# Performance work log

Measured on AMD Instinct MI355X. Metric: run time of the kernel, lower is better.

## Reference

```python
import jax, jax.numpy as jnp
import numpy as np

NUM_K_HEADS = 16
NUM_V_HEADS = 32
DK = 128
DV = 128
KCONV = 4
EPS = 1e-6
KEY_DIM = NUM_K_HEADS * DK      # 2048
VALUE_DIM = NUM_V_HEADS * DV    # 4096
HIDDEN = 2048
T_TOKENS = 4096


def setup_inputs() -> dict:
    key = jax.random.key(0)
    ks = jax.random.split(key, 10)
    s = 0.02
    return {
        "hidden_states": jax.random.normal(ks[0], (T_TOKENS, HIDDEN), jnp.float32),
        "W_qkv": jax.random.normal(ks[1], (2 * KEY_DIM + VALUE_DIM, HIDDEN), jnp.float32) * s,
        "W_z": jax.random.normal(ks[2], (VALUE_DIM, HIDDEN), jnp.float32) * s,
        "W_b": jax.random.normal(ks[3], (NUM_V_HEADS, HIDDEN), jnp.float32) * s,
        "W_a": jax.random.normal(ks[4], (NUM_V_HEADS, HIDDEN), jnp.float32) * s,
        "conv_weight": jax.random.normal(ks[5], (2 * KEY_DIM + VALUE_DIM, KCONV), jnp.float32) * 0.2,
        "dt_bias": jnp.ones((NUM_V_HEADS,), jnp.float32),
        "A_log": jax.random.normal(ks[6], (NUM_V_HEADS,), jnp.float32) * 0.5,
        "norm_weight": jnp.ones((DV,), jnp.float32),
        "W_out": jax.random.normal(ks[7], (HIDDEN, VALUE_DIM), jnp.float32) * s,
    }


def _l2norm(x):
    return x * jax.lax.rsqrt(jnp.sum(x * x, axis=-1, keepdims=True) + 1e-6)


def _gdn_forward(hidden_states, W_qkv, W_z, W_b, W_a, conv_weight,
                 dt_bias, A_log, norm_weight, W_out):
    T = hidden_states.shape[0]
    # input projections
    mixed_qkv = hidden_states @ W_qkv.T                         # [T, 2K+V]
    z = (hidden_states @ W_z.T).reshape(T, NUM_V_HEADS, DV)     # gate
    b = hidden_states @ W_b.T                                   # [T, Hv]
    a = hidden_states @ W_a.T                                   # [T, Hv]

    # depthwise causal conv1d (kernel 4) + silu, no bias
    xp = jnp.pad(mixed_qkv, ((KCONV - 1, 0), (0, 0)))
    conv = sum(xp[i:i + T] * conv_weight[:, i] for i in range(KCONV))
    x = jax.nn.silu(conv)

    q = x[:, :KEY_DIM].reshape(T, NUM_K_HEADS, DK)
    k = x[:, KEY_DIM:2 * KEY_DIM].reshape(T, NUM_K_HEADS, DK)
    v = x[:, 2 * KEY_DIM:].reshape(T, NUM_V_HEADS, DV)

    rep = NUM_V_HEADS // NUM_K_HEADS  # grouped value attention: repeat q/k heads
    q = jnp.repeat(_l2norm(q), rep, axis=1)  # [T, Hv, DK]
    k = jnp.repeat(_l2norm(k), rep, axis=1)

    beta = jax.nn.sigmoid(b)                                   # [T, Hv]
    g = -jnp.exp(A_log) * jax.nn.softplus(a + dt_bias)         # [T, Hv] log-decay
    scale = DK ** -0.5

    def step(S, inp):
        qt, kt, vt, bt, gt = inp
        S = S * jnp.exp(gt)[:, None, None]                     # gated decay
        kv = jnp.einsum('hk,hkv->hv', kt, S)                   # memory readout
        delta = (vt - kv) * bt[:, None]                        # delta rule update
        S = S + jnp.einsum('hk,hv->hkv', kt, delta)
        ot = jnp.einsum('hk,hkv->hv', qt, S) * scale
        return S, ot

    S0 = jnp.zeros((NUM_V_HEADS, DK, DV), mixed_qkv.dtype)
    _, o = jax.lax.scan(step, S0, (q, k, v, beta, g))          # o: [T, Hv, DV]

    # gated RMSNorm (norm before gate)
    var = jnp.mean(o * o, axis=-1, keepdims=True)
    on = o * jax.lax.rsqrt(var + EPS) * norm_weight
    y = on * jax.nn.silu(z)

    return y.reshape(T, VALUE_DIM) @ W_out.T                   # [T, HIDDEN]


def reference(hidden_states, W_qkv, W_z, W_b, W_a, conv_weight,
              dt_bias, A_log, norm_weight, W_out):
    return _gdn_forward(hidden_states, W_qkv, W_z, W_b, W_a, conv_weight,
                        dt_bias, A_log, norm_weight, W_out)
```

## Files before the change

### kernel.cpp

```cpp
#include <hip/hip_runtime.h>
#include <cstdint>
#include <cstddef>

typedef __bf16 bf16_t;
typedef __bf16 bf16x8 __attribute__((ext_vector_type(8)));
typedef __bf16 bf16x4 __attribute__((ext_vector_type(4)));
typedef float floatx4 __attribute__((ext_vector_type(4)));

__device__ __forceinline__ void async16(const bf16_t* g, bf16_t* l) {
  __builtin_amdgcn_global_load_lds(
      (const __attribute__((address_space(1))) unsigned int*)g,
      (__attribute__((address_space(3))) unsigned int*)l, 16, 0, 0);
}

__device__ __forceinline__ void barrier_lds() {
  asm volatile("s_waitcnt lgkmcnt(0)\n\ts_barrier" ::: "memory");
}

__device__ __forceinline__ float siluf(float x) { return x / (1.f + __expf(-x)); }

#define MFMA16(a, b, c) __builtin_amdgcn_mfma_f32_16x16x32_bf16(a, b, c, 0, 0, 0)

__global__ __launch_bounds__(256) void k_cvt(const float* __restrict__ in,
                                             bf16_t* __restrict__ out, int n4) {
  int i = blockIdx.x * 256 + threadIdx.x;
  if (i >= n4) return;
  const float4 f = ((const float4*)in)[i];
  bf16x4 r;
  r[0] = (bf16_t)f.x; r[1] = (bf16_t)f.y; r[2] = (bf16_t)f.z; r[3] = (bf16_t)f.w;
  ((bf16x4*)out)[i] = r;
}

__global__ __launch_bounds__(256) void k_build_wba(const float* __restrict__ wb,
                                                   const float* __restrict__ wa,
                                                   bf16_t* __restrict__ out) {
  int i = blockIdx.x * 256 + threadIdx.x;
  int e = i * 4;
  int row = e >> 11;
  int col = e & 2047;
  float4 f = make_float4(0.f, 0.f, 0.f, 0.f);
  if (row < 32)      f = *(const float4*)&wb[row * 2048 + col];
  else if (row < 64) f = *(const float4*)&wa[(row - 32) * 2048 + col];
  bf16x4 r;
  r[0] = (bf16_t)f.x; r[1] = (bf16_t)f.y; r[2] = (bf16_t)f.z; r[3] = (bf16_t)f.w;
  *(bf16x4*)&out[e] = r;
}

template<bool OUT_BF16>
__global__ __launch_bounds__(256) void gemm_bt(const bf16_t* __restrict__ A,
                                               const bf16_t* __restrict__ B,
                                               void* __restrict__ Cout,
                                               int M, int N, int K) {
  __shared__ __align__(16) bf16_t As[4096];
  __shared__ __align__(16) bf16_t Bs[4096];
  const int tid  = threadIdx.x;
  const int lane = tid & 63;
  const int wave = tid >> 6;
  const int quad = lane >> 4;
  const int l16  = lane & 15;
  const int wr   = (wave >> 1) * 64;
  const int wc   = (wave & 1) * 64;
  const int m0   = blockIdx.y * 128;
  const int n0   = blockIdx.x * 128;
  const int ra   = tid >> 2;
  const int ca   = (tid & 3) * 8;

  const bf16_t* gA = A + (size_t)(m0 + ra) * K + ca;
  const bf16_t* gB = B + (size_t)(n0 + ra) * K + ca;
  bf16_t* lA = &As[tid * 8];
  bf16_t* lB = &Bs[tid * 8];

  floatx4 acc[4][4] = {};

  for (int k0 = 0; k0 < K; k0 += 32) {
    __syncthreads();
    async16(gA + k0, lA);
    async16(gA + k0 + (size_t)64 * K, lA + 2048);
    async16(gB + k0, lB);
    async16(gB + k0 + (size_t)64 * K, lB + 2048);
    __syncthreads();
    bf16x8 af[4], bfr[4];
#pragma unroll
    for (int i = 0; i < 4; ++i) {
      af[i]  = *(const bf16x8*)&As[(wr + i * 16 + l16) * 32 + quad * 8];
      bfr[i] = *(const bf16x8*)&Bs[(wc + i * 16 + l16) * 32 + quad * 8];
    }
#pragma unroll
    for (int mi = 0; mi < 4; ++mi)
#pragma unroll
      for (int ni = 0; ni < 4; ++ni)
        acc[mi][ni] = MFMA16(af[mi], bfr[ni], acc[mi][ni]);
  }

#pragma unroll
  for (int mi = 0; mi < 4; ++mi) {
#pragma unroll
    for (int ni = 0; ni < 4; ++ni) {
      const int row = m0 + wr + mi * 16 + quad * 4;
      const int col = n0 + wc + ni * 16 + l16;
#pragma unroll
      for (int r = 0; r < 4; ++r) {
        if (OUT_BF16)
          ((bf16_t*)Cout)[(size_t)(row + r) * N + col] = (bf16_t)acc[mi][ni][r];
        else
          ((float*)Cout)[(size_t)(row + r) * N + col] = acc[mi][ni][r];
      }
    }
  }
}

template<bool OUT_BF16>
__global__ __launch_bounds__(512, 1) void gemm256(const bf16_t* __restrict__ A,
                                                  const bf16_t* __restrict__ B,
                                                  void* __restrict__ Cout,
                                                  int M, int N, int K) {
  extern __shared__ __align__(16) bf16_t sm[];
  const int tid  = threadIdx.x;
  const int lane = tid & 63;
  const int wave = tid >> 6;
  const int quad = lane >> 4;
  const int l16  = lane & 15;
  const int wm   = wave >> 2;
  const int wn   = wave & 3;

  const int gx  = (int)gridDim.x;
  const int nwg = gx * (int)gridDim.y;
  const int id  = (int)blockIdx.y * gx + (int)blockIdx.x;
  const int cpx = nwg >> 3;
  const int sw  = (id & 7) * cpx + (id >> 3);
  const int m0  = (sw / gx) * 256;
  const int n0  = (sw % gx) * 256;

  const int lr    = lane >> 2;
  const int lslot = (lane & 3) ^ ((lane >> 3) & 3);
  const bf16_t* gA = A + (size_t)(m0 + wave * 32 + lr) * K + lslot * 8;
  const bf16_t* gB = B + (size_t)(n0 + wave * 32 + lr) * K + lslot * 8;
  const int ldsA0 = wave * 1024 + lane * 8;
  const int ldsB0 = 8192 + wave * 1024 + lane * 8;

#define STG_A(u, kt) {                                          \
    bf16_t* la = sm + (u) * 16384 + ldsA0;                      \
    const bf16_t* ga = gA + (size_t)(kt) * 32;                  \
    async16(ga, la);                                            \
    async16(ga + (size_t)16 * K, la + 512); }
#define STG_B(u, kt) {                                          \
    bf16_t* lb = sm + (u) * 16384 + ldsB0;                      \
    const bf16_t* gb = gB + (size_t)(kt) * 32;                  \
    async16(gb, lb);                                            \
    async16(gb + (size_t)16 * K, lb + 512); }

  int offA[8], offB[4];
#pragma unroll
  for (int i = 0; i < 8; ++i) {
    int ra = wm * 128 + i * 16 + l16;
    offA[i] = (ra * 32 + quad * 8) ^ (((ra >> 1) & 3) << 3);
  }
#pragma unroll
  for (int i = 0; i < 4; ++i) {
    int rb = wn * 64 + i * 16 + l16;
    offB[i] = 8192 + ((rb * 32 + quad * 8) ^ (((rb >> 1) & 3) << 3));
  }

  floatx4 acc[8][4] = {};
  const int KT = K >> 5;

  STG_A(0, 0); STG_B(0, 0);
  STG_A(1, 1); STG_B(1, 1);
  STG_A(2, 2); STG_B(2, 2);
  asm volatile("s_waitcnt vmcnt(8)" ::: "memory");
  asm volatile("s_barrier" ::: "memory");

  for (int U = 0; U < KT; ++U) {
    const int bu = U & 3;
    const bf16_t* sb = sm + bu * 16384;
    const int un = U + 3;
    const int tu = un & 3;
    bf16x8 af[4], bfr[4];

#pragma unroll
    for (int i = 0; i < 4; ++i) {
      af[i]  = *(const bf16x8*)&sb[offA[i]];
      bfr[i] = *(const bf16x8*)&sb[offB[i]];
    }
    if (un < KT) STG_A(tu, un);
    asm volatile("s_barrier" ::: "memory");
    __builtin_amdgcn_s_setprio(1);
#pragma unroll
    for (int mi = 0; mi < 4; ++mi)
#pragma unroll
      for (int ni = 0; ni < 4; ++ni)
        acc[mi][ni] = MFMA16(af[mi], bfr[ni], acc[mi][ni]);
    __builtin_amdgcn_s_setprio(0);
    asm volatile("s_barrier" ::: "memory");

#pragma unroll
    for (int i = 0; i < 4; ++i) af[i] = *(const bf16x8*)&sb[offA[4 + i]];
    if (un < KT) STG_B(tu, un);
    if (un < KT)         asm volatile("s_waitcnt vmcnt(8)" ::: "memory");
    else if (U + 2 < KT) asm volatile("s_waitcnt vmcnt(4)" ::: "memory");
    else                 asm volatile("s_waitcnt vmcnt(0)" ::: "memory");
    asm volatile("s_barrier" ::: "memory");
    __builtin_amdgcn_s_setprio(1);
#pragma unroll
    for (int mi = 0; mi < 4; ++mi)
#pragma unroll
      for (int ni = 0; ni < 4; ++ni)
        acc[4 + mi][ni] = MFMA16(af[mi], bfr[ni], acc[4 + mi][ni]);
    __builtin_amdgcn_s_setprio(0);
    asm volatile("s_barrier" ::: "memory");
  }
#undef STG_A
#undef STG_B

#pragma unroll
  for (int mi = 0; mi < 8; ++mi) {
#pragma unroll
    for (int ni = 0; ni < 4; ++ni) {
      const int row = m0 + wm * 128 + mi * 16 + quad * 4;
      const int col = n0 + wn * 64 + ni * 16 + l16;
#pragma unroll
      for (int r = 0; r < 4; ++r) {
        if (OUT_BF16)
          ((bf16_t*)Cout)[(size_t)(row + r) * N + col] = (bf16_t)acc[mi][ni][r];
        else
          ((float*)Cout)[(size_t)(row + r) * N + col] = acc[mi][ni][r];
      }
    }
  }
}

__global__ __launch_bounds__(256) void k_betag(const float* __restrict__ cba,
                                               const float* __restrict__ A_log,
                                               const float* __restrict__ dtb,
                                               float* __restrict__ beta_t,
                                               float* __restrict__ g_t) {
  int i = blockIdx.x * 256 + threadIdx.x;
  int t = i >> 5, h = i & 31;
  float b = cba[t * 128 + h];
  float a = cba[t * 128 + 32 + h];
  beta_t[h * 4096 + t] = 1.f / (1.f + __expf(-b));
  float x = a + dtb[h];
  float sp = (x > 20.f) ? x : log1pf(__expf(x));
  g_t[h * 4096 + t] = -__expf(A_log[h]) * sp;
}

__global__ __launch_bounds__(64) void k_conv(const bf16_t* __restrict__ mixed,
                                             const float* __restrict__ cw,
                                             bf16_t* __restrict__ qo,
                                             bf16_t* __restrict__ ko,
                                             bf16_t* __restrict__ vo) {
  const int grp = blockIdx.x;
  const int t0 = blockIdx.y * 8;
  const int l = threadIdx.x;
  const int c0 = grp * 128 + l;
  const int c1 = c0 + 64;
  const float4 w0 = *(const float4*)&cw[c0 * 4];
  const float4 w1 = *(const float4*)&cw[c1 * 4];
  float h0[3], h1[3];
#pragma unroll
  for (int j = 0; j < 3; ++j) {
    int tt = t0 - 3 + j;
    h0[j] = (tt >= 0) ? (float)mixed[(size_t)tt * 8192 + c0] : 0.f;
    h1[j] = (tt >= 0) ? (float)mixed[(size_t)tt * 8192 + c1] : 0.f;
  }
#pragma unroll
  for (int i = 0; i < 8; ++i) {
    const int t = t0 + i;
    float x0 = (float)mixed[(size_t)t * 8192 + c0];
    float x1 = (float)mixed[(size_t)t * 8192 + c1];
    float a0 = w0.x * h0[0] + w0.y * h0[1] + w0.z * h0[2] + w0.w * x0;
    float a1 = w1.x * h1[0] + w1.y * h1[1] + w1.z * h1[2] + w1.w * x1;
    h0[0] = h0[1]; h0[1] = h0[2]; h0[2] = x0;
    h1[0] = h1[1]; h1[1] = h1[2]; h1[2] = x1;
    float v0 = siluf(a0), v1 = siluf(a1);
    if (grp < 32) {
      float s = v0 * v0 + v1 * v1;
#pragma unroll
      for (int m = 1; m < 64; m <<= 1) s += __shfl_xor(s, m);
      float r = rsqrtf(s + 1e-6f);
      if (grp < 16) {
        bf16_t* q = qo + ((size_t)t * 16 + grp) * 128;
        q[l]      = (bf16_t)(v0 * r * 0.08838834764831845f);
        q[l + 64] = (bf16_t)(v1 * r * 0.08838834764831845f);
      } else {
        bf16_t* k = ko + ((size_t)t * 16 + grp - 16) * 128;
        k[l]      = (bf16_t)(v0 * r);
        k[l + 64] = (bf16_t)(v1 * r);
      }
    } else {
      bf16_t* v = vo + ((size_t)t * 32 + grp - 32) * 128;
      v[l]      = (bf16_t)v0;
      v[l + 64] = (bf16_t)v1;
    }
  }
}

__global__ __launch_bounds__(256, 2) void k_prep(
    const bf16_t* __restrict__ qg, const bf16_t* __restrict__ kg,
    const bf16_t* __restrict__ vg,
    const float* __restrict__ bb_t, const float* __restrict__ gb_t,
    bf16_t* __restrict__ Vt, bf16_t* __restrict__ Wlo, bf16_t* __restrict__ Whi,
    bf16_t* __restrict__ Mout, bf16_t* __restrict__ kt, float* __restrict__ smalls) {
  const int c = blockIdx.x >> 5;
  const int h = blockIdx.x & 31;
  const int kh = h >> 1;
  const int t0 = c * 64;
  const int tid = threadIdx.x, lane = tid & 63, wave = tid >> 6;
  const int quad = lane >> 4, l16 = lane & 15;

  __shared__ __align__(16) bf16_t lsKQ[2][64][136];
  __shared__ float lsC[64][68];
  __shared__ float lsG[64], lsA[64], lsSc[64], lsBeta[64];

  {
    const int r = tid >> 2, s0 = (tid & 3) * 32;
    const bf16_t* kr = kg + ((size_t)(t0 + r) * 16 + kh) * 128 + s0;
    const bf16_t* qr = qg + ((size_t)(t0 + r) * 16 + kh) * 128 + s0;
#pragma unroll
    for (int j = 0; j < 4; ++j) {
      *(uint4*)&lsKQ[0][r][s0 + j * 8] = *(const uint4*)&kr[j * 8];
      *(uint4*)&lsKQ[1][r][s0 + j * 8] = *(const uint4*)&qr[j * 8];
    }
  }
  if (wave == 0) {
    float gv = gb_t[(size_t)h * 4096 + t0 + lane];
#pragma unroll
    for (int off = 1; off < 64; off <<= 1) {
      float n = __shfl_up(gv, off);
      if (lane >= off) gv += n;
    }
    float GL = __shfl(gv, 63);
    lsG[lane] = gv;
    lsA[lane] = __expf(gv);
    lsSc[lane] = __expf(GL - gv);
    lsBeta[lane] = bb_t[(size_t)h * 4096 + t0 + lane];
  }
  __syncthreads();

  const int mr = (wave >> 1) * 32, nr = (wave & 1) * 32;
  floatx4 ak[2][2] = {}, aq[2][2] = {};
  if (wave != 1) {
#pragma unroll
    for (int ks = 0; ks < 4; ++ks) {
      bf16x8 yf[2], xk[2], xq[2];
#pragma unroll
      for (int i = 0; i < 2; ++i) {
        yf[i] = *(const bf16x8*)&lsKQ[0][nr + i * 16 + l16][ks * 32 + quad * 8];
        xk[i] = *(const bf16x8*)&lsKQ[0][mr + i * 16 + l16][ks * 32 + quad * 8];
        xq[i] = *(const bf16x8*)&lsKQ[1][mr + i * 16 + l16][ks * 32 + quad * 8];
      }
#pragma unroll
      for (int i = 0; i < 2; ++i)
#pragma unroll
        for (int j = 0; j < 2; ++j) {
          ak[i][j] = MFMA16(xk[i], yf[j], ak[i][j]);
          aq[i][j] = MFMA16(xq[i], yf[j], aq[i][j]);
        }
    }
  }
  bf16_t* Mb = Mout + (size_t)(h * 64 + c) * 4096;
#pragma unroll
  for (int i = 0; i < 2; ++i)
#pragma unroll
    for (int j = 0; j < 2; ++j)
#pragma unroll
      for (int r = 0; r < 4; ++r) {
        int t = mr + i * 16 + quad * 4 + r;
        int s = nr + j * 16 + l16;
        float e = __expf(lsG[t] - lsG[s]);
        float cv = (s < t) ? lsBeta[t] * e * ak[i][j][r] : 0.f;
        float mv = (s <= t) ? e * aq[i][j][r] : 0.f;
        if (wave != 1) lsC[t][s] = cv;
        Mb[t * 64 + s] = (bf16_t)mv;
      }
  __syncthreads();

  const int col = tid & 127;
  const bool isW = tid >= 128;
  float vals[64];
#pragma unroll
  for (int t = 0; t < 64; ++t) {
    float b;
    if (!isW) b = (float)vg[((size_t)(t0 + t) * 32 + h) * 128 + col];
    else      b = lsA[t] * (float)lsKQ[0][t][col];
    vals[t] = lsBeta[t] * b;
  }
#pragma unroll
  for (int t = 1; t < 64; ++t) {
    float acc = vals[t];
#pragma unroll
    for (int s4 = 0; s4 <= (t - 1) >> 2; ++s4) {
      float4 cv = *(const float4*)&lsC[t][s4 * 4];
      acc -= cv.x * vals[s4 * 4 + 0];
      acc -= cv.y * vals[s4 * 4 + 1];
      acc -= cv.z * vals[s4 * 4 + 2];
      acc -= cv.w * vals[s4 * 4 + 3];
    }
    vals[t] = acc;
  }

  if (!isW) {
    bf16_t* vd = Vt + (size_t)(h * 64 + c) * 8192 + (size_t)col * 64;
#pragma unroll
    for (int j = 0; j < 16; ++j) {
      bf16x4 p;
      p[0] = (bf16_t)vals[j * 4 + 0];
      p[1] = (bf16_t)vals[j * 4 + 1];
      p[2] = (bf16_t)vals[j * 4 + 2];
      p[3] = (bf16_t)vals[j * 4 + 3];
      *(bf16x4*)&vd[j * 4] = p;
    }
  } else {
#pragma unroll
    for (int t = 0; t < 64; ++t) vals[t] = -vals[t];
  }

  if ((h & 1) == 0) {
    const int dk = tid >> 1, sh = (tid & 1) * 32;
    bf16_t* kd = kt + (size_t)(c * 16 + kh) * 8192 + (size_t)dk * 64 + sh;
#pragma unroll
    for (int j4 = 0; j4 < 4; ++j4) {
      bf16x8 v;
#pragma unroll
      for (int e = 0; e < 8; ++e) v[e] = lsKQ[0][sh + j4 * 8 + e][dk];
      *(bf16x8*)&kd[j4 * 8] = v;
    }
  }
  if (tid < 64) {
    float* sm = smalls + (size_t)(h * 64 + c) * 128;
    sm[tid] = lsA[tid];
    sm[64 + tid] = lsSc[tid];
  }
  __syncthreads();

  bf16_t* lsT = &lsKQ[0][0][0];
  if (isW) {
#pragma unroll
    for (int t = 0; t < 64; ++t) lsT[t * 272 + tid] = (bf16_t)vals[t];
  }
  __syncthreads();

  {
    const int r = tid >> 2, part = tid & 3;
    const bf16_t* src = &lsT[r * 272 + 128 + part * 32];
    bf16_t* Wb = (h < 16 ? Wlo : Whi) + (size_t)((h & 15) * 64 + c) * 8192 + r * 128 + part * 32;
#pragma unroll
    for (int j = 0; j < 4; ++j)
      *(uint4*)&Wb[j * 8] = *(const uint4*)&src[j * 8];
  }
}

__device__ __forceinline__ void chain_prefetch(
    int c2, int wave, int l16, int quad, int trow, int dv0, int kh,
    const bf16_t* __restrict__ Wbase, const bf16_t* __restrict__ Vbase,
    const bf16_t* __restrict__ Mbase, const bf16_t* __restrict__ qg,
    const bf16_t* __restrict__ ktg, const float* __restrict__ Sbase,
    bf16x8 nW[4], bf16x8 nQ[4], bf16x8 nK[4], bf16x8 nM[2],
    bf16x4 nV[4], float4& nA, float4& nSc, float& nAL) {
  const bf16_t* Wn = Wbase + (size_t)c2 * 8192;
  const bf16_t* Vn = Vbase + (size_t)c2 * 8192;
  const bf16_t* Qn = qg + ((size_t)(c2 * 64 + wave * 16 + l16) * 16 + kh) * 128;
  const bf16_t* Kn = ktg + (size_t)(c2 * 16 + kh) * 8192;
  const bf16_t* Mn = Mbase + (size_t)c2 * 4096 + (wave * 16 + l16) * 64;
  const float* sm = Sbase + (size_t)c2 * 128;
#pragma unroll
  for (int ks = 0; ks < 4; ++ks) {
    nW[ks] = *(const bf16x8*)&Wn[(size_t)(wave * 16 + l16) * 128 + ks * 32 + quad * 8];
    nQ[ks] = *(const bf16x8*)&Qn[ks * 32 + quad * 8];
    nK[ks] = *(const bf16x8*)&Kn[(size_t)((wave + 4 * (ks >> 1)) * 16 + l16) * 64 + (ks & 1) * 32 + quad * 8];
  }
#pragma unroll
  for (int ks = 0; ks < 2; ++ks) nM[ks] = *(const bf16x8*)&Mn[ks * 32 + quad * 8];
#pragma unroll
  for (int tn = 0; tn < 4; ++tn)
    nV[tn] = *(const bf16x4*)&Vn[(size_t)(dv0 + tn * 16 + l16) * 64 + trow];
  nA = *(const float4*)&sm[trow];
  nSc = *(const float4*)&sm[64 + trow];
  nAL = sm[63];
}

__global__ __launch_bounds__(256, 1) void k_chain(
    const bf16_t* __restrict__ qg, const bf16_t* __restrict__ VtT,
    const bf16_t* __restrict__ Wlo, const bf16_t* __restrict__ Whi,
    const bf16_t* __restrict__ Mg, const bf16_t* __restrict__ ktg,
    const float* __restrict__ smalls, bf16_t* __restrict__ o) {
  const int h = blockIdx.x & 31;
  const int dv0 = (blockIdx.x >> 5) * 64;
  const int kh = h >> 1;
  const int tid = threadIdx.x, lane = tid & 63, wave = tid >> 6;
  const int quad = lane >> 4, l16 = lane & 15;
  const int trow = wave * 16 + quad * 4;

  __shared__ __align__(16) bf16_t lsXT[64][72];
  __shared__ __align__(16) bf16_t lsXbT[64][72];
  __shared__ __align__(16) bf16_t lsS[64][136];

  const bf16_t* Wbase = (h < 16 ? Wlo : Whi) + (size_t)(h & 15) * 64 * 8192;
  const bf16_t* Vbase = VtT + (size_t)h * 64 * 8192;
  const bf16_t* Mbase = Mg + (size_t)h * 64 * 4096;
  const float*  Sbase = smalls + (size_t)h * 64 * 128;

  floatx4 sacc[2][4] = {};
  for (int i = tid; i < 64 * 136; i += 256) (&lsS[0][0])[i] = (bf16_t)0.f;

  bf16x8 nW[4], nQ[4], nK[4], nM[2];
  bf16x4 nV[4];
  float4 nA, nSc;
  float nAL;
  chain_prefetch(0, wave, l16, quad, trow, dv0, kh, Wbase, Vbase, Mbase, qg, ktg,
                 Sbase, nW, nQ, nK, nM, nV, nA, nSc, nAL);
  __syncthreads();

  for (int cc = 0; cc < 64; ++cc) {
    const int t0 = cc * 64;
    bf16x8 cW[4], cQ[4], cK[4], cM[2];
    float cV[16];
    float4 cA = nA, cSc = nSc;
    float cAL = nAL;
#pragma unroll
    for (int ks = 0; ks < 4; ++ks) { cW[ks] = nW[ks]; cQ[ks] = nQ[ks]; cK[ks] = nK[ks]; }
    cM[0] = nM[0]; cM[1] = nM[1];
#pragma unroll
    for (int tn = 0; tn < 4; ++tn)
#pragma unroll
      for (int r = 0; r < 4; ++r) cV[tn * 4 + r] = (float)nV[tn][r];

    if (cc + 1 < 64)
      chain_prefetch(cc + 1, wave, l16, quad, trow, dv0, kh, Wbase, Vbase, Mbase,
                     qg, ktg, Sbase, nW, nQ, nK, nM, nV, nA, nSc, nAL);

    bf16x8 bS[4][4];
#pragma unroll
    for (int ks = 0; ks < 4; ++ks)
#pragma unroll
      for (int tn = 0; tn < 4; ++tn)
        bS[ks][tn] = *(const bf16x8*)&lsS[tn * 16 + l16][ks * 32 + quad * 8];
    floatx4 xacc[4];
#pragma unroll
    for (int tn = 0; tn < 4; ++tn)
#pragma unroll
      for (int r = 0; r < 4; ++r) xacc[tn][r] = cV[tn * 4 + r];
#pragma unroll
    for (int ks = 0; ks < 4; ++ks)
#pragma unroll
      for (int tn = 0; tn < 4; ++tn)
        xacc[tn] = MFMA16(cW[ks], bS[ks][tn], xacc[tn]);
#pragma unroll
    for (int tn = 0; tn < 4; ++tn) {
      bf16x4 px, pb;
#pragma unroll
      for (int r = 0; r < 4; ++r) {
        px[r] = (bf16_t)xacc[tn][r];
        pb[r] = (bf16_t)(xacc[tn][r] * ((const float*)&cSc)[r]);
      }
      *(bf16x4*)&lsXT[tn * 16 + l16][trow] = px;
      *(bf16x4*)&lsXbT[tn * 16 + l16][trow] = pb;
    }
    barrier_lds();

    floatx4 qacc[4] = {};
#pragma unroll
    for (int ks = 0; ks < 4; ++ks)
#pragma unroll
      for (int tn = 0; tn < 4; ++tn)
        qacc[tn] = MFMA16(cQ[ks], bS[ks][tn], qacc[tn]);
#pragma unroll
    for (int tn = 0; tn < 4; ++tn)
#pragma unroll
      for (int r = 0; r < 4; ++r) qacc[tn][r] *= ((const float*)&cA)[r];
#pragma unroll
    for (int ks = 0; ks < 2; ++ks)
#pragma unroll
      for (int tn = 0; tn < 4; ++tn) {
        bf16x8 bX = *(const bf16x8*)&lsXT[tn * 16 + l16][ks * 32 + quad * 8];
        qacc[tn] = MFMA16(cM[ks], bX, qacc[tn]);
      }
#pragma unroll
    for (int tn = 0; tn < 4; ++tn)
#pragma unroll
      for (int r = 0; r < 4; ++r)
        o[((size_t)(t0 + trow + r) * 32 + h) * 128 + dv0 + tn * 16 + l16] =
            (bf16_t)qacc[tn][r];
#pragma unroll
    for (int mh = 0; mh < 2; ++mh)
#pragma unroll
      for (int tn = 0; tn < 4; ++tn)
#pragma unroll
        for (int r = 0; r < 4; ++r) sacc[mh][tn][r] *= cAL;
#pragma unroll
    for (int ks = 0; ks < 2; ++ks) {
      bf16x8 bXb[4];
#pragma unroll
      for (int tn = 0; tn < 4; ++tn)
        bXb[tn] = *(const bf16x8*)&lsXbT[tn * 16 + l16][ks * 32 + quad * 8];
#pragma unroll
      for (int mh = 0; mh < 2; ++mh)
#pragma unroll
        for (int tn = 0; tn < 4; ++tn)
          sacc[mh][tn] = MFMA16(cK[mh * 2 + ks], bXb[tn], sacc[mh][tn]);
    }
#pragma unroll
    for (int mh = 0; mh < 2; ++mh)
#pragma unroll
      for (int tn = 0; tn < 4; ++tn) {
        bf16x4 ps;
#pragma unroll
        for (int r = 0; r < 4; ++r) ps[r] = (bf16_t)sacc[mh][tn][r];
        *(bf16x4*)&lsS[tn * 16 + l16][(wave + 4 * mh) * 16 + quad * 4] = ps;
      }
    barrier_lds();
  }
}

__global__ __launch_bounds__(256) void k_gate(const bf16_t* __restrict__ o,
                                              const bf16_t* __restrict__ z,
                                              const float* __restrict__ nw,
                                              bf16_t* __restrict__ y) {
  const int row = blockIdx.x * 4 + (threadIdx.x >> 6);
  const int l = threadIdx.x & 63;
  const bf16_t* orow = o + (size_t)row * 128;
  float o0 = (float)orow[l], o1 = (float)orow[l + 64];
  float s = o0 * o0 + o1 * o1;
#pragma unroll
  for (int m = 1; m < 64; m <<= 1) s += __shfl_xor(s, m);
  float r = rsqrtf(s * (1.f / 128.f) + 1e-6f);
  const bf16_t* zrow = z + (size_t)row * 128;
  float z0 = (float)zrow[l], z1 = (float)zrow[l + 64];
  bf16_t* yrow = y + (size_t)row * 128;
  yrow[l]      = (bf16_t)(o0 * r * nw[l] * siluf(z0));
  yrow[l + 64] = (bf16_t)(o1 * r * nw[l + 64] * siluf(z1));
}

extern "C" void kernel_launch(void* const* d_in, const int* in_sizes, int n_in,
                              void* d_out, int out_size, void* d_ws, size_t ws_size,
                              hipStream_t stream) {
  const float* hidden = (const float*)d_in[0];
  const float* W_qkv  = (const float*)d_in[1];
  const float* W_z    = (const float*)d_in[2];
  const float* W_b    = (const float*)d_in[3];
  const float* W_a    = (const float*)d_in[4];
  const float* conv_w = (const float*)d_in[5];
  const float* dt_b   = (const float*)d_in[6];
  const float* A_log  = (const float*)d_in[7];
  const float* norm_w = (const float*)d_in[8];
  const float* W_out  = (const float*)d_in[9];
  float* out = (float*)d_out;

  static int gemm_attr_done = 0;
  if (!gemm_attr_done) {
    hipFuncSetAttribute(reinterpret_cast<const void*>(&gemm256<true>),
                        hipFuncAttributeMaxDynamicSharedMemorySize, 131072);
    hipFuncSetAttribute(reinterpret_cast<const void*>(&gemm256<false>),
                        hipFuncAttributeMaxDynamicSharedMemorySize, 131072);
    gemm_attr_done = 1;
  }

  char* w = (char*)d_ws;
  const size_t MB = 1024 * 1024;
  bf16_t* hs    = (bf16_t*)(w + 0 * MB);
  bf16_t* Wlo   = hs;
  bf16_t* wqkv  = (bf16_t*)(w + 16 * MB);
  bf16_t* Vtb   = wqkv;
  bf16_t* ybuf  = wqkv;
  bf16_t* wz    = (bf16_t*)(w + 48 * MB);
  bf16_t* Whi   = wz;
  bf16_t* wout  = (bf16_t*)(w + 64 * MB);
  bf16_t* wba   = (bf16_t*)(w + 80 * MB);
  bf16_t* mixed = (bf16_t*)(w + 81 * MB);
  bf16_t* obuf  = mixed;
  bf16_t* Mbuf  = (bf16_t*)(w + 113 * MB);
  bf16_t* ktb   = (bf16_t*)(w + 129 * MB);
  bf16_t* zbuf  = (bf16_t*)(w + 145 * MB);
  float*  cba   = (float*)(w + 177 * MB);
  float*  smalls= cba;
  bf16_t* qb    = (bf16_t*)(w + 179 * MB);
  bf16_t* kb    = (bf16_t*)(w + 195 * MB);
  bf16_t* vb    = (bf16_t*)(w + 211 * MB);
  float*  betab = (float*)(w + 243 * MB);
  float*  gbuf  = (float*)(w + 243 * MB + 512 * 1024);

  k_cvt<<<8192, 256, 0, stream>>>(hidden, hs, 2097152);
  k_cvt<<<16384, 256, 0, stream>>>(W_qkv, wqkv, 4194304);
  k_cvt<<<8192, 256, 0, stream>>>(W_z, wz, 2097152);
  k_cvt<<<8192, 256, 0, stream>>>(W_out, wout, 2097152);
  k_build_wba<<<256, 256, 0, stream>>>(W_b, W_a, wba);

  gemm256<true><<<dim3(32, 16), 512, 131072, stream>>>(hs, wqkv, mixed, 4096, 8192, 2048);
  gemm256<true><<<dim3(16, 16), 512, 131072, stream>>>(hs, wz, zbuf, 4096, 4096, 2048);
  gemm_bt<false><<<dim3(1, 32), 256, 0, stream>>>(hs, wba, cba, 4096, 128, 2048);
  k_betag<<<512, 256, 0, stream>>>(cba, A_log, dt_b, betab, gbuf);

  k_conv<<<dim3(64, 512), 64, 0, stream>>>(mixed, conv_w, qb, kb, vb);

  k_prep<<<2048, 256, 0, stream>>>(qb, kb, vb, betab, gbuf,
                                   Vtb, Wlo, Whi, Mbuf, ktb, smalls);
  k_chain<<<64, 256, 0, stream>>>(qb, Vtb, Wlo, Whi, Mbuf, ktb, smalls, obuf);

  k_gate<<<32768, 256, 0, stream>>>(obuf, zbuf, norm_w, ybuf);
  gemm_bt<false><<<dim3(16, 32), 256, 0, stream>>>(ybuf, wout, out, 4096, 2048, 4096);
}
```

Before: 904.3 us.

## Use pointer-increment prefetch in chain, reorder barrier, use 256-tile GEMM for output

The chain kernel's prefetch helper is inlined and now uses running pointers that advance each chunk, replacing the per-iteration address recomputation. The decay scaling of the state accumulator moves ahead of the LDS barrier so it can overlap with the barrier wait. The output projection switches from gemm_bt to the larger 256-tile gemm256 kernel with 512 threads, aiming for better data reuse in the final GEMM, though it launches fewer blocks (128 instead of 512).

```diff
diff --git a/kernel.cpp b/kernel.cpp
--- a/kernel.cpp
+++ b/kernel.cpp
@@ -450,35 +450,6 @@
   }
 }
 
-__device__ __forceinline__ void chain_prefetch(
-    int c2, int wave, int l16, int quad, int trow, int dv0, int kh,
-    const bf16_t* __restrict__ Wbase, const bf16_t* __restrict__ Vbase,
-    const bf16_t* __restrict__ Mbase, const bf16_t* __restrict__ qg,
-    const bf16_t* __restrict__ ktg, const float* __restrict__ Sbase,
-    bf16x8 nW[4], bf16x8 nQ[4], bf16x8 nK[4], bf16x8 nM[2],
-    bf16x4 nV[4], float4& nA, float4& nSc, float& nAL) {
-  const bf16_t* Wn = Wbase + (size_t)c2 * 8192;
-  const bf16_t* Vn = Vbase + (size_t)c2 * 8192;
-  const bf16_t* Qn = qg + ((size_t)(c2 * 64 + wave * 16 + l16) * 16 + kh) * 128;
-  const bf16_t* Kn = ktg + (size_t)(c2 * 16 + kh) * 8192;
-  const bf16_t* Mn = Mbase + (size_t)c2 * 4096 + (wave * 16 + l16) * 64;
-  const float* sm = Sbase + (size_t)c2 * 128;
-#pragma unroll
-  for (int ks = 0; ks < 4; ++ks) {
-    nW[ks] = *(const bf16x8*)&Wn[(size_t)(wave * 16 + l16) * 128 + ks * 32 + quad * 8];
-    nQ[ks] = *(const bf16x8*)&Qn[ks * 32 + quad * 8];
-    nK[ks] = *(const bf16x8*)&Kn[(size_t)((wave + 4 * (ks >> 1)) * 16 + l16) * 64 + (ks & 1) * 32 + quad * 8];
-  }
-#pragma unroll
-  for (int ks = 0; ks < 2; ++ks) nM[ks] = *(const bf16x8*)&Mn[ks * 32 + quad * 8];
-#pragma unroll
-  for (int tn = 0; tn < 4; ++tn)
-    nV[tn] = *(const bf16x4*)&Vn[(size_t)(dv0 + tn * 16 + l16) * 64 + trow];
-  nA = *(const float4*)&sm[trow];
-  nSc = *(const float4*)&sm[64 + trow];
-  nAL = sm[63];
-}
-
 __global__ __launch_bounds__(256, 1) void k_chain(
     const bf16_t* __restrict__ qg, const bf16_t* __restrict__ VtT,
     const bf16_t* __restrict__ Wlo, const bf16_t* __restrict__ Whi,
@@ -500,6 +471,13 @@
   const bf16_t* Mbase = Mg + (size_t)h * 64 * 4096;
   const float*  Sbase = smalls + (size_t)h * 64 * 128;
 
+  const bf16_t* pW = Wbase + (size_t)(wave * 16 + l16) * 128 + quad * 8;
+  const bf16_t* pQ = qg + ((size_t)(wave * 16 + l16) * 16 + kh) * 128 + quad * 8;
+  const bf16_t* pK = ktg + (size_t)kh * 8192 + (size_t)(wave * 16 + l16) * 64 + quad * 8;
+  const bf16_t* pM = Mbase + (size_t)(wave * 16 + l16) * 64 + quad * 8;
+  const bf16_t* pV = Vbase + (size_t)(dv0 + l16) * 64 + trow;
+  const float*  pS = Sbase;
+
   floatx4 sacc[2][4] = {};
   for (int i = tid; i < 64 * 136; i += 256) (&lsS[0][0])[i] = (bf16_t)0.f;
 
@@ -507,8 +485,25 @@
   bf16x4 nV[4];
   float4 nA, nSc;
   float nAL;
-  chain_prefetch(0, wave, l16, quad, trow, dv0, kh, Wbase, Vbase, Mbase, qg, ktg,
-                 Sbase, nW, nQ, nK, nM, nV, nA, nSc, nAL);
+  {
+#pragma unroll
+    for (int ks = 0; ks < 4; ++ks) {
+      nW[ks] = *(const bf16x8*)&pW[ks * 32];
+      nQ[ks] = *(const bf16x8*)&pQ[ks * 32];
+    }
+    nK[0] = *(const bf16x8*)&pK[0];
+    nK[1] = *(const bf16x8*)&pK[32];
+    nK[2] = *(const bf16x8*)&pK[4096];
+    nK[3] = *(const bf16x8*)&pK[4096 + 32];
+    nM[0] = *(const bf16x8*)&pM[0];
+    nM[1] = *(const bf16x8*)&pM[32];
+#pragma unroll
+    for (int tn = 0; tn < 4; ++tn) nV[tn] = *(const bf16x4*)&pV[tn * 1024];
+    nA  = *(const float4*)&pS[trow];
+    nSc = *(const float4*)&pS[64 + trow];
+    nAL = pS[63];
+    pW += 8192; pQ += 131072; pK += 131072; pM += 4096; pV += 8192; pS += 128;
+  }
   __syncthreads();
 
   for (int cc = 0; cc < 64; ++cc) {
@@ -525,9 +520,25 @@
 #pragma unroll
       for (int r = 0; r < 4; ++r) cV[tn * 4 + r] = (float)nV[tn][r];
 
-    if (cc + 1 < 64)
-      chain_prefetch(cc + 1, wave, l16, quad, trow, dv0, kh, Wbase, Vbase, Mbase,
-                     qg, ktg, Sbase, nW, nQ, nK, nM, nV, nA, nSc, nAL);
+    if (cc + 1 < 64) {
+#pragma unroll
+      for (int ks = 0; ks < 4; ++ks) {
+        nW[ks] = *(const bf16x8*)&pW[ks * 32];
+        nQ[ks] = *(const bf16x8*)&pQ[ks * 32];
+      }
+      nK[0] = *(const bf16x8*)&pK[0];
+      nK[1] = *(const bf16x8*)&pK[32];
+      nK[2] = *(const bf16x8*)&pK[4096];
+      nK[3] = *(const bf16x8*)&pK[4096 + 32];
+      nM[0] = *(const bf16x8*)&pM[0];
+      nM[1] = *(const bf16x8*)&pM[32];
+#pragma unroll
+      for (int tn = 0; tn < 4; ++tn) nV[tn] = *(const bf16x4*)&pV[tn * 1024];
+      nA  = *(const float4*)&pS[trow];
+      nSc = *(const float4*)&pS[64 + trow];
+      nAL = pS[63];
+      pW += 8192; pQ += 131072; pK += 131072; pM += 4096; pV += 8192; pS += 128;
+    }
 
     bf16x8 bS[4][4];
 #pragma unroll
@@ -556,8 +567,6 @@
       *(bf16x4*)&lsXT[tn * 16 + l16][trow] = px;
       *(bf16x4*)&lsXbT[tn * 16 + l16][trow] = pb;
     }
-    barrier_lds();
-
     floatx4 qacc[4] = {};
 #pragma unroll
     for (int ks = 0; ks < 4; ++ks)
@@ -568,6 +577,14 @@
     for (int tn = 0; tn < 4; ++tn)
 #pragma unroll
       for (int r = 0; r < 4; ++r) qacc[tn][r] *= ((const float*)&cA)[r];
+#pragma unroll
+    for (int mh = 0; mh < 2; ++mh)
+#pragma unroll
+      for (int tn = 0; tn < 4; ++tn)
+#pragma unroll
+        for (int r = 0; r < 4; ++r) sacc[mh][tn][r] *= cAL;
+    barrier_lds();
+
 #pragma unroll
     for (int ks = 0; ks < 2; ++ks)
 #pragma unroll
@@ -581,12 +598,7 @@
       for (int r = 0; r < 4; ++r)
         o[((size_t)(t0 + trow + r) * 32 + h) * 128 + dv0 + tn * 16 + l16] =
             (bf16_t)qacc[tn][r];
-#pragma unroll
-    for (int mh = 0; mh < 2; ++mh)
-#pragma unroll
-      for (int tn = 0; tn < 4; ++tn)
-#pragma unroll
-        for (int r = 0; r < 4; ++r) sacc[mh][tn][r] *= cAL;
+
 #pragma unroll
     for (int ks = 0; ks < 2; ++ks) {
       bf16x8 bXb[4];
@@ -697,5 +709,5 @@
   k_chain<<<64, 256, 0, stream>>>(qb, Vtb, Wlo, Whi, Mbuf, ktb, smalls, obuf);
 
   k_gate<<<32768, 256, 0, stream>>>(obuf, zbuf, norm_w, ybuf);
-  gemm_bt<false><<<dim3(16, 32), 256, 0, stream>>>(ybuf, wout, out, 4096, 2048, 4096);
-}
+  gemm256<false><<<dim3(8, 16), 512, 131072, stream>>>(ybuf, wout, out, 4096, 2048, 4096);
+}
```

Measured after the change: 901.2 us. No clear change (-0.3%).
